# Optimization experiments

Hardware: AMD Instinct MI355X
Metric: run time of the kernel (lower is better)

Reference implementation:

```python
import jax, jax.numpy as jnp
import numpy as np

N_NODES = 100000
N_EDGES = 1600000


def _lin_init(k, din, dout):
    # xavier-normal-ish weight, zero bias handled separately
    s = (2.0 / (din + dout)) ** 0.5
    return jax.random.normal(k, (din, dout), jnp.float32) * s


def setup_inputs() -> dict:
    key = jax.random.key(0)
    ks = jax.random.split(key, 32)
    inp = {
        "node_feat": jax.random.normal(ks[0], (N_NODES, 3), jnp.float32),
        "edge_feat": jax.random.normal(ks[1], (N_EDGES, 1), jnp.float32),
        "edge_dist": jax.random.normal(ks[2], (N_EDGES, 1), jnp.float32),
        "src": jax.random.randint(ks[3], (N_EDGES,), 0, N_NODES),
        "dst": jax.random.randint(ks[4], (N_EDGES,), 0, N_NODES),
    }
    dims = {"enc": [3, 64, 64, 8], "dec": [8, 64, 64, 1],
            "nod": [9, 64, 64, 8], "edg": [17, 64, 64, 1]}
    i = 5
    for name, d in dims.items():
        for l in range(3):
            inp[f"w_{name}{l+1}"] = _lin_init(ks[i], d[l], d[l + 1]); i += 1
            inp[f"b_{name}{l+1}"] = jnp.zeros((d[l + 1],), jnp.float32)
    return inp


def _mlp(x, w1, b1, w2, b2, w3, b3):
    x = jax.nn.relu(x @ w1 + b1)
    x = jax.nn.relu(x @ w2 + b2)
    return jax.nn.relu(x @ w3 + b3)


def _edge_softmax(dist, dst, n):
    # softmax over incoming edges per destination node (DGL edge_softmax)
    m = jax.ops.segment_max(dist, dst, num_segments=n)          # [N,1]
    e = jnp.exp(dist - m[dst])                                   # [E,1]
    s = jax.ops.segment_sum(e, dst, num_segments=n)              # [N,1]
    return e / s[dst]


def reference(node_feat, edge_feat, edge_dist, src, dst,
              w_enc1, b_enc1, w_enc2, b_enc2, w_enc3, b_enc3,
              w_dec1, b_dec1, w_dec2, b_dec2, w_dec3, b_dec3,
              w_nod1, b_nod1, w_nod2, b_nod2, w_nod3, b_nod3,
              w_edg1, b_edg1, w_edg2, b_edg2, w_edg3, b_edg3):
    n = node_feat.shape[0]
    # encoder: [N,3] -> [N,8]
    h = _mlp(node_feat, w_enc1, b_enc1, w_enc2, b_enc2, w_enc3, b_enc3)
    # softmax-weighted aggregation of src features to dst
    w = _edge_softmax(edge_dist, dst, n)                         # [E,1]
    h = jax.ops.segment_sum(w * h[src], dst, num_segments=n)     # [N,8]
    he = edge_feat                                               # [E,1]
    for _ in range(2):
        x = jnp.concatenate([he, h[src], h[dst]], axis=-1)       # [E,17]
        he = _mlp(x, w_edg1, b_edg1, w_edg2, b_edg2, w_edg3, b_edg3)  # [E,1]
        agg = jax.ops.segment_sum(he, dst, num_segments=n)       # [N,1]
        h = _mlp(jnp.concatenate([agg, h], axis=-1),
                 w_nod1, b_nod1, w_nod2, b_nod2, w_nod3, b_nod3)  # [N,8]
    # second softmax aggregation (same dist -> same weights)
    h = jax.ops.segment_sum(w * h[src], dst, num_segments=n)     # [N,8]
    # decoder: [N,8] -> [N,1]
    return _mlp(h, w_dec1, b_dec1, w_dec2, b_dec2, w_dec3, b_dec3)
```

## Files before the change

### kernel.cpp

```cpp
#include <hip/hip_runtime.h>

#define N_NODES 100000
#define N_EDGES 1600000

typedef __attribute__((ext_vector_type(4))) float f32x4;
typedef __attribute__((ext_vector_type(8))) short bf16x8;

__device__ __forceinline__ unsigned short f2bf(float v) {
    unsigned u = __float_as_uint(v);
    unsigned r = (u + 0x7FFFu + ((u >> 16) & 1u)) >> 16;
    return (unsigned short)r;
}
__device__ __forceinline__ float bf2f(unsigned short h) {
    return __uint_as_float(((unsigned)h) << 16);
}

__global__ void zero_kernel(float* p, int n) {
    int i = blockIdx.x * blockDim.x + threadIdx.x;
    int stride = gridDim.x * blockDim.x;
    for (; i < n; i += stride) p[i] = 0.f;
}

__global__ void exp_sum_kernel(const float* __restrict__ dist, const int* __restrict__ dst,
                               float* __restrict__ s, float* __restrict__ wbuf, int E) {
    int e = blockIdx.x * blockDim.x + threadIdx.x;
    if (e >= E) return;
    float v = expf(dist[e]);
    wbuf[e] = v;
    atomicAdd(s + dst[e], v);
}

template <bool NORM>
__global__ void agg_kernel(float* wbuf, const float* __restrict__ s,
                           const float* __restrict__ hfeat,
                           const int* __restrict__ src, const int* __restrict__ dst,
                           float* __restrict__ out, int E) {
    int t = blockIdx.x * blockDim.x + threadIdx.x;
    if (t >= E * 8) return;
    int e = t >> 3, c = t & 7;
    float w = wbuf[e];
    int d = dst[e];
    if (NORM) {
        w = w / s[d];
        if (c == 0) wbuf[e] = w;
    }
    atomicAdd(out + d * 8 + c, w * hfeat[src[e] * 8 + c]);
}

struct PackArgs { const float *w1, *b1, *w2; float* out; int din, stride; };

__global__ void pack_kernel(PackArgs a0, PackArgs a1, PackArgs a2) {
    PackArgs a = (blockIdx.x == 0) ? a0 : (blockIdx.x == 1) ? a1 : a2;
    int k = threadIdx.x;
    float* row = a.out + k * a.stride;
    for (int j = 0; j < 64; ++j) row[j] = a.w2[k * 64 + j];
    for (int j = 0; j < a.din; ++j) row[64 + j] = a.w1[j * 64 + k];
    row[64 + a.din] = a.b1[k];
}

__global__ void pack_edge_kernel(const float* __restrict__ w1, const float* __restrict__ w2,
                                 unsigned short* __restrict__ w1hi, unsigned short* __restrict__ w1lo,
                                 unsigned short* __restrict__ w2hi, unsigned short* __restrict__ w2lo) {
    int c = threadIdx.x;
    for (int j = 0; j < 32; ++j) {
        float v = (j < 17) ? w1[j * 64 + c] : 0.f;
        unsigned short hi = f2bf(v);
        w1hi[c * 32 + j] = hi;
        w1lo[c * 32 + j] = f2bf(v - bf2f(hi));
    }
    for (int k = 0; k < 64; ++k) {
        float v = w2[k * 64 + c];
        unsigned short hi = f2bf(v);
        w2hi[c * 64 + k] = hi;
        w2lo[c * 64 + k] = f2bf(v - bf2f(hi));
    }
}

template <int DIN, int DOUT, int STRIDE>
__device__ __forceinline__ void mlp_fused(
    const float* __restrict__ x, const float* __restrict__ wp,
    const float* __restrict__ b2,
    const float* __restrict__ w3, const float* __restrict__ b3,
    float* __restrict__ out) {
    float h2[64];
#pragma unroll
    for (int j = 0; j < 64; ++j) h2[j] = b2[j];
    for (int k = 0; k < 64; ++k) {
        const float* row = wp + k * STRIDE;
        float a = row[64 + DIN];
#pragma unroll
        for (int j = 0; j < DIN; ++j) a = fmaf(x[j], row[64 + j], a);
        a = fmaxf(a, 0.f);
#pragma unroll
        for (int j = 0; j < 64; ++j) h2[j] = fmaf(a, row[j], h2[j]);
    }
    float acc[DOUT];
#pragma unroll
    for (int o = 0; o < DOUT; ++o) acc[o] = b3[o];
#pragma unroll
    for (int j = 0; j < 64; ++j) {
        float r = fmaxf(h2[j], 0.f);
#pragma unroll
        for (int o = 0; o < DOUT; ++o) acc[o] = fmaf(r, w3[j * DOUT + o], acc[o]);
    }
#pragma unroll
    for (int o = 0; o < DOUT; ++o) out[o] = fmaxf(acc[o], 0.f);
}

template <int CA, int CB, int DOUT, int STRIDE>
__global__ __launch_bounds__(256, 3) void node_mlp_kernel(
    const float* __restrict__ xa, const float* __restrict__ xb,
    const float* __restrict__ wp, const float* __restrict__ b2,
    const float* __restrict__ w3, const float* __restrict__ b3,
    float* __restrict__ out, int n) {
    constexpr int DIN = CA + CB;
    int i = blockIdx.x * 256 + threadIdx.x;
    if (i >= n) return;
    float x[DIN];
#pragma unroll
    for (int k = 0; k < CA; ++k) x[k] = xa[i * CA + k];
    if (CB == 8) {
        float4 v0 = *(const float4*)(xb + i * 8);
        float4 v1 = *(const float4*)(xb + i * 8 + 4);
        x[CA + 0] = v0.x; x[CA + 1] = v0.y; x[CA + 2] = v0.z; x[CA + 3] = v0.w;
        x[CA + 4] = v1.x; x[CA + 5] = v1.y; x[CA + 6] = v1.z; x[CA + 7] = v1.w;
    }
    float o[DOUT];
    mlp_fused<DIN, DOUT, STRIDE>(x, wp, b2, w3, b3, o);
#pragma unroll
    for (int k = 0; k < DOUT; ++k) out[i * DOUT + k] = o[k];
}

__global__ __launch_bounds__(128, 2) void edge_mlp_mfma_kernel(
    const float* __restrict__ he_in, const float* __restrict__ h,
    const int* __restrict__ src, const int* __restrict__ dst,
    const unsigned short* __restrict__ w1hi, const unsigned short* __restrict__ w1lo,
    const unsigned short* __restrict__ w2hi, const unsigned short* __restrict__ w2lo,
    const float* __restrict__ b1, const float* __restrict__ b2,
    const float* __restrict__ w3, const float* __restrict__ b3,
    float* __restrict__ he_out, float* __restrict__ agg) {
    __shared__ __align__(16) unsigned char smem[2 * 18432];
    const int lane = threadIdx.x & 63, wv = threadIdx.x >> 6;
    unsigned char* W = smem + wv * 18432;
    const int ebase = (blockIdx.x * 2 + wv) * 64;

    {
        int e = ebase + lane;
        float x[32];
        x[0] = he_in[e];
        int sr = src[e], dd = dst[e];
        float4 a0 = *(const float4*)(h + sr * 8);
        float4 a1 = *(const float4*)(h + sr * 8 + 4);
        float4 d0 = *(const float4*)(h + dd * 8);
        float4 d1 = *(const float4*)(h + dd * 8 + 4);
        x[1] = a0.x;  x[2] = a0.y;  x[3] = a0.z;  x[4] = a0.w;
        x[5] = a1.x;  x[6] = a1.y;  x[7] = a1.z;  x[8] = a1.w;
        x[9] = d0.x;  x[10] = d0.y; x[11] = d0.z; x[12] = d0.w;
        x[13] = d1.x; x[14] = d1.y; x[15] = d1.z; x[16] = d1.w;
#pragma unroll
        for (int j = 17; j < 32; ++j) x[j] = 0.f;
        unsigned uh[16], ul[16];
#pragma unroll
        for (int jj = 0; jj < 16; ++jj) {
            unsigned short h0 = f2bf(x[2 * jj]);
            unsigned short h1v = f2bf(x[2 * jj + 1]);
            unsigned short l0 = f2bf(x[2 * jj] - bf2f(h0));
            unsigned short l1 = f2bf(x[2 * jj + 1] - bf2f(h1v));
            uh[jj] = (unsigned)h0 | ((unsigned)h1v << 16);
            ul[jj] = (unsigned)l0 | ((unsigned)l1 << 16);
        }
        uint4* ph = (uint4*)(W + lane * 80);
        uint4* pl = (uint4*)(W + 5120 + lane * 80);
#pragma unroll
        for (int q = 0; q < 4; ++q) {
            ph[q] = make_uint4(uh[4 * q], uh[4 * q + 1], uh[4 * q + 2], uh[4 * q + 3]);
            pl[q] = make_uint4(ul[4 * q], ul[4 * q + 1], ul[4 * q + 2], ul[4 * q + 3]);
        }
    }
    __syncthreads();
    const int row = lane & 15, g = lane >> 4;

    bf16x8 wa_h[4], wa_l[4];
#pragma unroll
    for (int mt = 0; mt < 4; ++mt) {
        wa_h[mt] = *(const bf16x8*)(w1hi + (16 * mt + row) * 32 + g * 8);
        wa_l[mt] = *(const bf16x8*)(w1lo + (16 * mt + row) * 32 + g * 8);
    }
    bf16x8 xb_h[4], xb_l[4];
#pragma unroll
    for (int nt = 0; nt < 4; ++nt) {
        xb_h[nt] = *(const bf16x8*)(W + (16 * nt + row) * 80 + g * 16);
        xb_l[nt] = *(const bf16x8*)(W + 5120 + (16 * nt + row) * 80 + g * 16);
    }
    f32x4 c1[4][4];
#pragma unroll
    for (int mt = 0; mt < 4; ++mt)
#pragma unroll
        for (int nt = 0; nt < 4; ++nt) {
            f32x4 c = {0.f, 0.f, 0.f, 0.f};
            c = __builtin_amdgcn_mfma_f32_16x16x32_bf16(wa_h[mt], xb_h[nt], c, 0, 0, 0);
            c = __builtin_amdgcn_mfma_f32_16x16x32_bf16(wa_h[mt], xb_l[nt], c, 0, 0, 0);
            c = __builtin_amdgcn_mfma_f32_16x16x32_bf16(wa_l[mt], xb_h[nt], c, 0, 0, 0);
            c1[mt][nt] = c;
        }
    float4 b1v[4];
#pragma unroll
    for (int mt = 0; mt < 4; ++mt) b1v[mt] = *(const float4*)(b1 + 16 * mt + g * 4);
#pragma unroll
    for (int mt = 0; mt < 4; ++mt)
#pragma unroll
        for (int nt = 0; nt < 4; ++nt) {
            int el = 16 * nt + row;
            int ch0 = 16 * mt + g * 4;
            float v0 = fmaxf(c1[mt][nt].x + b1v[mt].x, 0.f);
            float v1 = fmaxf(c1[mt][nt].y + b1v[mt].y, 0.f);
            float v2 = fmaxf(c1[mt][nt].z + b1v[mt].z, 0.f);
            float v3 = fmaxf(c1[mt][nt].w + b1v[mt].w, 0.f);
            unsigned short h0 = f2bf(v0), h1v = f2bf(v1), h2v = f2bf(v2), h3 = f2bf(v3);
            unsigned hh0 = (unsigned)h0 | ((unsigned)h1v << 16);
            unsigned hh1 = (unsigned)h2v | ((unsigned)h3 << 16);
            unsigned ll0 = (unsigned)f2bf(v0 - bf2f(h0)) | ((unsigned)f2bf(v1 - bf2f(h1v)) << 16);
            unsigned ll1 = (unsigned)f2bf(v2 - bf2f(h2v)) | ((unsigned)f2bf(v3 - bf2f(h3)) << 16);
            *(uint2*)(W + el * 144 + ch0 * 2) = make_uint2(hh0, hh1);
            *(uint2*)(W + 9216 + el * 144 + ch0 * 2) = make_uint2(ll0, ll1);
        }
    __syncthreads();

    bf16x8 w2a_h[4][2], w2a_l[4][2];
#pragma unroll
    for (int mt = 0; mt < 4; ++mt)
#pragma unroll
        for (int ks = 0; ks < 2; ++ks) {
            w2a_h[mt][ks] = *(const bf16x8*)(w2hi + (16 * mt + row) * 64 + ks * 32 + g * 8);
            w2a_l[mt][ks] = *(const bf16x8*)(w2lo + (16 * mt + row) * 64 + ks * 32 + g * 8);
        }
    f32x4 c2[4][4];
#pragma unroll
    for (int mt = 0; mt < 4; ++mt)
#pragma unroll
        for (int nt = 0; nt < 4; ++nt) c2[mt][nt] = (f32x4){0.f, 0.f, 0.f, 0.f};
#pragma unroll
    for (int nt = 0; nt < 4; ++nt) {
        bf16x8 hb_h[2], hb_l[2];
#pragma unroll
        for (int ks = 0; ks < 2; ++ks) {
            hb_h[ks] = *(const bf16x8*)(W + (16 * nt + row) * 144 + (ks * 32 + g * 8) * 2);
            hb_l[ks] = *(const bf16x8*)(W + 9216 + (16 * nt + row) * 144 + (ks * 32 + g * 8) * 2);
        }
#pragma unroll
        for (int mt = 0; mt < 4; ++mt)
#pragma unroll
            for (int ks = 0; ks < 2; ++ks) {
                c2[mt][nt] = __builtin_amdgcn_mfma_f32_16x16x32_bf16(w2a_h[mt][ks], hb_h[ks], c2[mt][nt], 0, 0, 0);
                c2[mt][nt] = __builtin_amdgcn_mfma_f32_16x16x32_bf16(w2a_h[mt][ks], hb_l[ks], c2[mt][nt], 0, 0, 0);
                c2[mt][nt] = __builtin_amdgcn_mfma_f32_16x16x32_bf16(w2a_l[mt][ks], hb_h[ks], c2[mt][nt], 0, 0, 0);
            }
    }

    float4 b2v[4], w3v[4];
#pragma unroll
    for (int mt = 0; mt < 4; ++mt) {
        b2v[mt] = *(const float4*)(b2 + 16 * mt + g * 4);
        w3v[mt] = *(const float4*)(w3 + 16 * mt + g * 4);
    }
    float b3s = b3[0];
    float pacc[4];
#pragma unroll
    for (int nt = 0; nt < 4; ++nt) {
        float p = 0.f;
#pragma unroll
        for (int mt = 0; mt < 4; ++mt) {
            p = fmaf(fmaxf(c2[mt][nt].x + b2v[mt].x, 0.f), w3v[mt].x, p);
            p = fmaf(fmaxf(c2[mt][nt].y + b2v[mt].y, 0.f), w3v[mt].y, p);
            p = fmaf(fmaxf(c2[mt][nt].z + b2v[mt].z, 0.f), w3v[mt].z, p);
            p = fmaf(fmaxf(c2[mt][nt].w + b2v[mt].w, 0.f), w3v[mt].w, p);
        }
        p += __shfl_xor(p, 16);
        p += __shfl_xor(p, 32);
        pacc[nt] = p;
    }
    if (lane < 16) {
#pragma unroll
        for (int nt = 0; nt < 4; ++nt) {
            int e2 = ebase + 16 * nt + lane;
            float o = fmaxf(pacc[nt] + b3s, 0.f);
            he_out[e2] = o;
            atomicAdd(agg + dst[e2], o);
        }
    }
}

extern "C" void kernel_launch(void* const* d_in, const int* in_sizes, int n_in,
                              void* d_out, int out_size, void* d_ws, size_t ws_size,
                              hipStream_t stream) {
    const int N = N_NODES, E = N_EDGES;
    const float* node_feat = (const float*)d_in[0];
    const float* edge_feat = (const float*)d_in[1];
    const float* edge_dist = (const float*)d_in[2];
    const int* src = (const int*)d_in[3];
    const int* dst = (const int*)d_in[4];
    const float* w_enc1 = (const float*)d_in[5];  const float* b_enc1 = (const float*)d_in[6];
    const float* w_enc2 = (const float*)d_in[7];  const float* b_enc2 = (const float*)d_in[8];
    const float* w_enc3 = (const float*)d_in[9];  const float* b_enc3 = (const float*)d_in[10];
    const float* w_dec1 = (const float*)d_in[11]; const float* b_dec1 = (const float*)d_in[12];
    const float* w_dec2 = (const float*)d_in[13]; const float* b_dec2 = (const float*)d_in[14];
    const float* w_dec3 = (const float*)d_in[15]; const float* b_dec3 = (const float*)d_in[16];
    const float* w_nod1 = (const float*)d_in[17]; const float* b_nod1 = (const float*)d_in[18];
    const float* w_nod2 = (const float*)d_in[19]; const float* b_nod2 = (const float*)d_in[20];
    const float* w_nod3 = (const float*)d_in[21]; const float* b_nod3 = (const float*)d_in[22];
    const float* w_edg1 = (const float*)d_in[23]; const float* b_edg1 = (const float*)d_in[24];
    const float* w_edg2 = (const float*)d_in[25]; const float* b_edg2 = (const float*)d_in[26];
    const float* w_edg3 = (const float*)d_in[27]; const float* b_edg3 = (const float*)d_in[28];

    float* ws = (float*)d_ws;
    float* s      = ws;
    float* hagg1  = ws + N;
    float* agg1   = ws + 9 * N;
    float* agg2   = ws + 10 * N;
    float* hagg2  = ws + 11 * N;
    float* h_enc  = ws + 19 * N;
    float* h_r1   = ws + 27 * N;
    float* h_r2   = ws + 35 * N;
    float* wbuf   = ws + 43 * N;
    float* he1    = wbuf + E;
    float* he2    = he1 + E;
    float* pk_enc = he2 + E;
    float* pk_nod = pk_enc + 64 * 80;
    float* pk_dec = pk_nod + 64 * 80;
    unsigned short* w1hi = (unsigned short*)(pk_dec + 64 * 80);
    unsigned short* w1lo = w1hi + 64 * 32;
    unsigned short* w2hi = w1lo + 64 * 32;
    unsigned short* w2lo = w2hi + 64 * 64;

    PackArgs pa0{w_enc1, b_enc1, w_enc2, pk_enc, 3, 80};
    PackArgs pa1{w_nod1, b_nod1, w_nod2, pk_nod, 9, 80};
    PackArgs pa2{w_dec1, b_dec1, w_dec2, pk_dec, 8, 80};
    pack_kernel<<<3, 64, 0, stream>>>(pa0, pa1, pa2);
    pack_edge_kernel<<<1, 64, 0, stream>>>(w_edg1, w_edg2, w1hi, w1lo, w2hi, w2lo);

    zero_kernel<<<2048, 256, 0, stream>>>(ws, 19 * N);
    node_mlp_kernel<3, 0, 8, 80><<<(N + 255) / 256, 256, 0, stream>>>(node_feat, nullptr,
        pk_enc, b_enc2, w_enc3, b_enc3, h_enc, N);
    exp_sum_kernel<<<(E + 255) / 256, 256, 0, stream>>>(edge_dist, dst, s, wbuf, E);
    agg_kernel<true><<<(E * 8 + 255) / 256, 256, 0, stream>>>(wbuf, s, h_enc, src, dst, hagg1, E);
    edge_mlp_mfma_kernel<<<E / 128, 128, 0, stream>>>(edge_feat, hagg1, src, dst,
        w1hi, w1lo, w2hi, w2lo, b_edg1, b_edg2, w_edg3, b_edg3, he1, agg1);
    node_mlp_kernel<1, 8, 8, 80><<<(N + 255) / 256, 256, 0, stream>>>(agg1, hagg1,
        pk_nod, b_nod2, w_nod3, b_nod3, h_r1, N);
    edge_mlp_mfma_kernel<<<E / 128, 128, 0, stream>>>(he1, h_r1, src, dst,
        w1hi, w1lo, w2hi, w2lo, b_edg1, b_edg2, w_edg3, b_edg3, he2, agg2);
    node_mlp_kernel<1, 8, 8, 80><<<(N + 255) / 256, 256, 0, stream>>>(agg2, h_r1,
        pk_nod, b_nod2, w_nod3, b_nod3, h_r2, N);
    agg_kernel<false><<<(E * 8 + 255) / 256, 256, 0, stream>>>(wbuf, s, h_r2, src, dst, hagg2, E);
    node_mlp_kernel<8, 0, 1, 80><<<(N + 255) / 256, 256, 0, stream>>>(hagg2, nullptr,
        pk_dec, b_dec2, w_dec3, b_dec3, (float*)d_out, N);
}
```

Measured before the change: 798.4 us.

## Feed layer-1 MFMA outputs directly as layer-2 operands via permuted W2 packing

Instead of writing the hidden layer (hi/lo bf16 split) to shared memory and reading it back as B operands, the kernel builds the B fragments in registers directly from the layer-1 accumulators. W2 is packed in a permuted K order so that the register layout of the accumulator matches the MFMA operand layout. This removes the LDS round trip and a __syncthreads, and shrinks shared memory, at the cost of more live registers.

```diff
diff --git a/kernel.cpp b/kernel.cpp
--- a/kernel.cpp
+++ b/kernel.cpp
@@ -68,11 +68,16 @@
         w1hi[c * 32 + j] = hi;
         w1lo[c * 32 + j] = f2bf(v - bf2f(hi));
     }
-    for (int k = 0; k < 64; ++k) {
-        float v = w2[k * 64 + c];
+    int mt = c >> 4, row = c & 15;
+    for (int ch = 0; ch < 64; ++ch) {
+        int ks = ch >> 5, r5 = ch & 31;
+        int i = ((r5 >> 4) << 2) | (r5 & 3);
+        int g = (r5 >> 2) & 3;
+        int dstIdx = (((mt * 2 + ks) * 16 + row) * 4 + g) * 8 + i;
+        float v = w2[ch * 64 + c];
         unsigned short hi = f2bf(v);
-        w2hi[c * 64 + k] = hi;
-        w2lo[c * 64 + k] = f2bf(v - bf2f(hi));
+        w2hi[dstIdx] = hi;
+        w2lo[dstIdx] = f2bf(v - bf2f(hi));
     }
 }
 
@@ -139,9 +144,9 @@
     const float* __restrict__ b1, const float* __restrict__ b2,
     const float* __restrict__ w3, const float* __restrict__ b3,
     float* __restrict__ he_out, float* __restrict__ agg) {
-    __shared__ __align__(16) unsigned char smem[2 * 18432];
+    __shared__ __align__(16) unsigned char smem[2 * 10240];
     const int lane = threadIdx.x & 63, wv = threadIdx.x >> 6;
-    unsigned char* W = smem + wv * 18432;
+    unsigned char* W = smem + wv * 10240;
     const int ebase = (blockIdx.x * 2 + wv) * 64;
 
     {
@@ -203,57 +208,57 @@
             c = __builtin_amdgcn_mfma_f32_16x16x32_bf16(wa_l[mt], xb_h[nt], c, 0, 0, 0);
             c1[mt][nt] = c;
         }
+
     float4 b1v[4];
 #pragma unroll
     for (int mt = 0; mt < 4; ++mt) b1v[mt] = *(const float4*)(b1 + 16 * mt + g * 4);
+    bf16x8 pb_h[4][2], pb_l[4][2];
+#pragma unroll
+    for (int nt = 0; nt < 4; ++nt)
+#pragma unroll
+        for (int ks = 0; ks < 2; ++ks) {
+            float v0 = fmaxf(c1[2 * ks][nt].x + b1v[2 * ks].x, 0.f);
+            float v1 = fmaxf(c1[2 * ks][nt].y + b1v[2 * ks].y, 0.f);
+            float v2 = fmaxf(c1[2 * ks][nt].z + b1v[2 * ks].z, 0.f);
+            float v3 = fmaxf(c1[2 * ks][nt].w + b1v[2 * ks].w, 0.f);
+            float v4 = fmaxf(c1[2 * ks + 1][nt].x + b1v[2 * ks + 1].x, 0.f);
+            float v5 = fmaxf(c1[2 * ks + 1][nt].y + b1v[2 * ks + 1].y, 0.f);
+            float v6 = fmaxf(c1[2 * ks + 1][nt].z + b1v[2 * ks + 1].z, 0.f);
+            float v7 = fmaxf(c1[2 * ks + 1][nt].w + b1v[2 * ks + 1].w, 0.f);
+            unsigned short h0 = f2bf(v0), h1v = f2bf(v1), h2v = f2bf(v2), h3 = f2bf(v3);
+            unsigned short h4 = f2bf(v4), h5 = f2bf(v5), h6 = f2bf(v6), h7 = f2bf(v7);
+            bf16x8 ph, pl;
+            ph[0] = h0; ph[1] = h1v; ph[2] = h2v; ph[3] = h3;
+            ph[4] = h4; ph[5] = h5;  ph[6] = h6;  ph[7] = h7;
+            pl[0] = f2bf(v0 - bf2f(h0)); pl[1] = f2bf(v1 - bf2f(h1v));
+            pl[2] = f2bf(v2 - bf2f(h2v)); pl[3] = f2bf(v3 - bf2f(h3));
+            pl[4] = f2bf(v4 - bf2f(h4)); pl[5] = f2bf(v5 - bf2f(h5));
+            pl[6] = f2bf(v6 - bf2f(h6)); pl[7] = f2bf(v7 - bf2f(h7));
+            pb_h[nt][ks] = ph;
+            pb_l[nt][ks] = pl;
+        }
+
+    f32x4 c2[4][4];
 #pragma unroll
     for (int mt = 0; mt < 4; ++mt)
 #pragma unroll
-        for (int nt = 0; nt < 4; ++nt) {
-            int el = 16 * nt + row;
-            int ch0 = 16 * mt + g * 4;
-            float v0 = fmaxf(c1[mt][nt].x + b1v[mt].x, 0.f);
-            float v1 = fmaxf(c1[mt][nt].y + b1v[mt].y, 0.f);
-            float v2 = fmaxf(c1[mt][nt].z + b1v[mt].z, 0.f);
-            float v3 = fmaxf(c1[mt][nt].w + b1v[mt].w, 0.f);
-            unsigned short h0 = f2bf(v0), h1v = f2bf(v1), h2v = f2bf(v2), h3 = f2bf(v3);
-            unsigned hh0 = (unsigned)h0 | ((unsigned)h1v << 16);
-            unsigned hh1 = (unsigned)h2v | ((unsigned)h3 << 16);
-            unsigned ll0 = (unsigned)f2bf(v0 - bf2f(h0)) | ((unsigned)f2bf(v1 - bf2f(h1v)) << 16);
-            unsigned ll1 = (unsigned)f2bf(v2 - bf2f(h2v)) | ((unsigned)f2bf(v3 - bf2f(h3)) << 16);
-            *(uint2*)(W + el * 144 + ch0 * 2) = make_uint2(hh0, hh1);
-            *(uint2*)(W + 9216 + el * 144 + ch0 * 2) = make_uint2(ll0, ll1);
-        }
-    __syncthreads();
-
-    bf16x8 w2a_h[4][2], w2a_l[4][2];
-#pragma unroll
-    for (int mt = 0; mt < 4; ++mt)
+        for (int nt = 0; nt < 4; ++nt) c2[mt][nt] = (f32x4){0.f, 0.f, 0.f, 0.f};
+#pragma unroll
+    for (int mt = 0; mt < 4; ++mt) {
+        bf16x8 w2a_h[2], w2a_l[2];
 #pragma unroll
         for (int ks = 0; ks < 2; ++ks) {
-            w2a_h[mt][ks] = *(const bf16x8*)(w2hi + (16 * mt + row) * 64 + ks * 32 + g * 8);
-            w2a_l[mt][ks] = *(const bf16x8*)(w2lo + (16 * mt + row) * 64 + ks * 32 + g * 8);
-        }
-    f32x4 c2[4][4];
-#pragma unroll
-    for (int mt = 0; mt < 4; ++mt)
-#pragma unroll
-        for (int nt = 0; nt < 4; ++nt) c2[mt][nt] = (f32x4){0.f, 0.f, 0.f, 0.f};
-#pragma unroll
-    for (int nt = 0; nt < 4; ++nt) {
-        bf16x8 hb_h[2], hb_l[2];
-#pragma unroll
-        for (int ks = 0; ks < 2; ++ks) {
-            hb_h[ks] = *(const bf16x8*)(W + (16 * nt + row) * 144 + (ks * 32 + g * 8) * 2);
-            hb_l[ks] = *(const bf16x8*)(W + 9216 + (16 * nt + row) * 144 + (ks * 32 + g * 8) * 2);
-        }
-#pragma unroll
-        for (int mt = 0; mt < 4; ++mt)
+            int off = (((mt * 2 + ks) * 16 + row) * 4 + g) * 8;
+            w2a_h[ks] = *(const bf16x8*)(w2hi + off);
+            w2a_l[ks] = *(const bf16x8*)(w2lo + off);
+        }
+#pragma unroll
+        for (int nt = 0; nt < 4; ++nt)
 #pragma unroll
             for (int ks = 0; ks < 2; ++ks) {
-                c2[mt][nt] = __builtin_amdgcn_mfma_f32_16x16x32_bf16(w2a_h[mt][ks], hb_h[ks], c2[mt][nt], 0, 0, 0);
-                c2[mt][nt] = __builtin_amdgcn_mfma_f32_16x16x32_bf16(w2a_h[mt][ks], hb_l[ks], c2[mt][nt], 0, 0, 0);
-                c2[mt][nt] = __builtin_amdgcn_mfma_f32_16x16x32_bf16(w2a_l[mt][ks], hb_h[ks], c2[mt][nt], 0, 0, 0);
+                c2[mt][nt] = __builtin_amdgcn_mfma_f32_16x16x32_bf16(w2a_h[ks], pb_h[nt][ks], c2[mt][nt], 0, 0, 0);
+                c2[mt][nt] = __builtin_amdgcn_mfma_f32_16x16x32_bf16(w2a_h[ks], pb_l[nt][ks], c2[mt][nt], 0, 0, 0);
+                c2[mt][nt] = __builtin_amdgcn_mfma_f32_16x16x32_bf16(w2a_l[ks], pb_h[nt][ks], c2[mt][nt], 0, 0, 0);
             }
     }
 
```

New measurement: 721.4 us. -9.6%, faster.
